# Optimization experiments

Measured on AMD Instinct MI355X. Metric: run time of the kernel, lower is better.

The kernel has to match this reference:

```python
import jax, jax.numpy as jnp
import numpy as np

B, N, D = 8, 8192, 3

def setup_inputs() -> dict:
    key = jax.random.key(0)
    k1, k2 = jax.random.split(key)
    adv_pc = jax.random.normal(k1, (B, N, D), dtype=jnp.float32)
    ori_pc = jax.random.normal(k2, (B, N, D), dtype=jnp.float32)
    weights = jnp.ones((B,), dtype=jnp.float32)
    return {"adv_pc": adv_pc, "ori_pc": ori_pc, "weights": weights}

def _batch_pairwise_dist(x, y):
    # x: [B, Nx, D], y: [B, Ny, D] -> P: [B, Nx, Ny]
    rx = jnp.sum(x * x, axis=-1)                      # [B, Nx]
    ry = jnp.sum(y * y, axis=-1)                      # [B, Ny]
    zz = jnp.einsum('bnd,bmd->bnm', x, y)             # [B, Nx, Ny]
    return rx[:, :, None] + ry[:, None, :] - 2.0 * zz

def reference(adv_pc, ori_pc, weights):
    # chamfer(preds=adv_pc, gts=ori_pc): P = pairwise(ori, adv) -> [B, N_ori, N_adv]
    P = _batch_pairwise_dist(ori_pc, adv_pc)
    loss1 = jnp.mean(jnp.min(P, axis=1), axis=1)      # adv2ori: for each adv pt, nearest ori
    # method == 'adv2ori' -> loss = loss1
    loss = loss1 * weights
    return jnp.mean(loss)
```

## Files before the change

### kernel.cpp

```cpp
#include <hip/hip_runtime.h>
#include <float.h>

#define NB 8
#define NPTS 8192
#define TOTAL (NB * NPTS)
#define BLK 256
#define WAVES 4
#define GROUPS 8
#define ADV_PER_WAVE (GROUPS * 32)
#define ADV_PER_BLOCK (WAVES * ADV_PER_WAVE)
#define ADV_BLOCKS (TOTAL / ADV_PER_BLOCK)
#define OSPLIT 16
#define OSLICE (NPTS / OSPLIT)
#define REC_SHORTS 16
#define GRID_MAIN (ADV_BLOCKS * OSPLIT)
#define BF16_ONE 0x3F80

typedef short short8 __attribute__((ext_vector_type(8)));
typedef float floatx16 __attribute__((ext_vector_type(16)));

__device__ __forceinline__ unsigned short f2bf(float f) {
    unsigned int u = __float_as_uint(f);
    return (unsigned short)((u + 0x7FFFu + ((u >> 16) & 1u)) >> 16);
}
__device__ __forceinline__ float bf2f(unsigned short h) {
    return __uint_as_float(((unsigned int)h) << 16);
}
__device__ __forceinline__ float min3(float a, float b, float c) {
    return fminf(fminf(a, b), c);
}
__device__ __forceinline__ float fold16(floatx16 d, float um) {
    float t0 = min3(d[0], d[1], d[2]);
    float t1 = min3(d[3], d[4], d[5]);
    float t2 = min3(d[6], d[7], d[8]);
    float t3 = min3(d[9], d[10], d[11]);
    float t4 = min3(d[12], d[13], d[14]);
    float t5 = min3(t0, t1, d[15]);
    float t6 = min3(t2, t3, t4);
    return min3(t5, t6, um);
}

__global__ __launch_bounds__(BLK, 4) void chamfer_mfma(const float* __restrict__ adv,
                                                       const float* __restrict__ ori,
                                                       float* __restrict__ partial) {
    __shared__ __align__(16) unsigned short lrec[OSLICE * REC_SHORTS];
    const int tid = threadIdx.x;
    const int wave = tid >> 6, lane = tid & 63;
    const int n32 = lane & 31, half = lane >> 5;
    const int advBlk = blockIdx.x >> 4;
    const int split = blockIdx.x & 15;
    const int b = advBlk >> 3;
    const int advLocal = (advBlk & 7) * ADV_PER_BLOCK + wave * ADV_PER_WAVE;

    {
        const float* orib = ori + (size_t)(b * NPTS + split * OSLICE) * 3;
#pragma unroll
        for (int r = 0; r < 2; r++) {
            int p = tid * 2 + r;
            float x = orib[3 * p + 0], y = orib[3 * p + 1], z = orib[3 * p + 2];
            unsigned short hx = f2bf(x), hy = f2bf(y), hz = f2bf(z);
            unsigned short lx = f2bf(x - bf2f(hx));
            unsigned short ly = f2bf(y - bf2f(hy));
            unsigned short lz = f2bf(z - bf2f(hz));
            float ro = fmaf(x, x, fmaf(y, y, z * z));
            unsigned short rh = f2bf(ro), rl = f2bf(ro - bf2f(rh));
            __align__(16) unsigned short rec[16] = {hx, hy, hz, lx, ly, lz, hx, hy,
                                                    hz, rh, rl, 0, 0, 0, 0, 0};
            float4* dst = (float4*)&lrec[p * REC_SHORTS];
            dst[0] = ((float4*)rec)[0];
            dst[1] = ((float4*)rec)[1];
        }
    }

    short8 bfr[GROUPS];
    float ra[GROUPS], um[GROUPS];
    const float* advb = adv + (size_t)b * NPTS * 3;
#pragma unroll
    for (int g = 0; g < GROUPS; g++) {
        int j = advLocal + g * 32 + n32;
        float x = advb[3 * j + 0], y = advb[3 * j + 1], z = advb[3 * j + 2];
        ra[g] = fmaf(x, x, fmaf(y, y, z * z));
        um[g] = FLT_MAX;
        unsigned short hx = f2bf(x), hy = f2bf(y), hz = f2bf(z);
        float fhx = bf2f(hx), fhy = bf2f(hy), fhz = bf2f(hz);
        unsigned short nhx = f2bf(-2.0f * fhx), nhy = f2bf(-2.0f * fhy), nhz = f2bf(-2.0f * fhz);
        unsigned short nlx = f2bf(-2.0f * bf2f(f2bf(x - fhx)));
        unsigned short nly = f2bf(-2.0f * bf2f(f2bf(y - fhy)));
        unsigned short nlz = f2bf(-2.0f * bf2f(f2bf(z - fhz)));
        __align__(16) unsigned short e[8] = {0, 0, 0, 0, 0, 0, 0, 0};
        if (half == 0) {
            e[0] = nhx; e[1] = nhy; e[2] = nhz;
            e[3] = nhx; e[4] = nhy; e[5] = nhz;
            e[6] = nlx; e[7] = nly;
        } else {
            e[0] = nlz; e[1] = BF16_ONE; e[2] = BF16_ONE;
        }
        bfr[g] = *(short8*)e;
    }
    __syncthreads();

    const floatx16 zero = {0.f, 0.f, 0.f, 0.f, 0.f, 0.f, 0.f, 0.f,
                           0.f, 0.f, 0.f, 0.f, 0.f, 0.f, 0.f, 0.f};
    const int lsh = n32 * REC_SHORTS + half * 8;

#pragma unroll 2
    for (int t = 0; t < OSLICE / 32; t++) {
        short8 af = *(const short8*)&lrec[t * 32 * REC_SHORTS + lsh];
#pragma unroll
        for (int g = 0; g < GROUPS; g++) {
            floatx16 d = __builtin_amdgcn_mfma_f32_32x32x16_bf16(af, bfr[g], zero, 0, 0, 0);
            um[g] = fold16(d, um[g]);
        }
    }

#pragma unroll
    for (int g = 0; g < GROUPS; g++) {
        float v = fminf(um[g], __shfl_xor(um[g], 32, 64));
        if (half == 0) {
            int col = b * NPTS + advLocal + g * 32 + n32;
            partial[(size_t)split * TOTAL + col] = ra[g] + v;
        }
    }
}

__global__ __launch_bounds__(BLK) void reduce_mins(const float* __restrict__ partial,
                                                   const float* __restrict__ w,
                                                   float* __restrict__ out) {
    const float4* p4 = (const float4*)partial;
    int g4 = blockIdx.x * BLK + threadIdx.x;
    float4 m = p4[g4];
#pragma unroll
    for (int s = 1; s < OSPLIT; s++) {
        float4 v = p4[(size_t)s * (TOTAL / 4) + g4];
        m.x = fminf(m.x, v.x); m.y = fminf(m.y, v.y);
        m.z = fminf(m.z, v.z); m.w = fminf(m.w, v.w);
    }
    float v = ((m.x + m.y) + (m.z + m.w)) * w[g4 >> 11];

    __shared__ float red[BLK];
    red[threadIdx.x] = v;
    __syncthreads();
    for (int s = BLK / 2; s > 0; s >>= 1) {
        if (threadIdx.x < s) red[threadIdx.x] += red[threadIdx.x + s];
        __syncthreads();
    }
    if (threadIdx.x == 0) atomicAdd(out, red[0] * (1.0f / (float)TOTAL));
}

extern "C" void kernel_launch(void* const* d_in, const int* in_sizes, int n_in,
                              void* d_out, int out_size, void* d_ws, size_t ws_size,
                              hipStream_t stream) {
    const float* adv = (const float*)d_in[0];
    const float* ori = (const float*)d_in[1];
    const float* w   = (const float*)d_in[2];
    float* out = (float*)d_out;
    float* partial = (float*)d_ws;

    hipMemsetAsync(out, 0, sizeof(float), stream);
    hipLaunchKernelGGL(chamfer_mfma, dim3(GRID_MAIN), dim3(BLK), 0, stream,
                       adv, ori, partial);
    hipLaunchKernelGGL(reduce_mins, dim3(TOTAL / 4 / BLK), dim3(BLK), 0, stream,
                       partial, w, out);
}
```

Before: 80.57 us.

## Drop memset, stage ori/adv loads via float4 into LDS, wave-shuffle reduce

Several changes land together. The separate memset is removed and the output is zeroed inside the main kernel. Half the block loads ori with float4 reads while the other half stages the adv block into LDS, and the adv fragments are then built from LDS. The reduce kernel shrinks to 64-thread blocks that sum with wave shuffles instead of an LDS tree. Together these aim to cut launch overhead, uncoalesced loads and synchronisation, at the cost of extra LDS use and an ordering assumption that block 0 zeroes the output before the next kernel's atomics.

```diff
diff --git a/kernel.cpp b/kernel.cpp
--- a/kernel.cpp
+++ b/kernel.cpp
@@ -42,22 +42,29 @@
 
 __global__ __launch_bounds__(BLK, 4) void chamfer_mfma(const float* __restrict__ adv,
                                                        const float* __restrict__ ori,
-                                                       float* __restrict__ partial) {
+                                                       float* __restrict__ partial,
+                                                       float* __restrict__ out) {
     __shared__ __align__(16) unsigned short lrec[OSLICE * REC_SHORTS];
+    __shared__ __align__(16) float advS[ADV_PER_BLOCK * 3];
     const int tid = threadIdx.x;
     const int wave = tid >> 6, lane = tid & 63;
     const int n32 = lane & 31, half = lane >> 5;
     const int advBlk = blockIdx.x >> 4;
     const int split = blockIdx.x & 15;
     const int b = advBlk >> 3;
-    const int advLocal = (advBlk & 7) * ADV_PER_BLOCK + wave * ADV_PER_WAVE;
+    const int advLocal = (advBlk & 7) * ADV_PER_BLOCK;
 
-    {
-        const float* orib = ori + (size_t)(b * NPTS + split * OSLICE) * 3;
+    if (blockIdx.x == 0 && tid == 0) out[0] = 0.0f;
+
+    if (tid < 128) {
+        const float4* op = (const float4*)(ori + (size_t)(b * NPTS + split * OSLICE) * 3);
+        float4 f0 = op[tid * 3 + 0], f1 = op[tid * 3 + 1], f2 = op[tid * 3 + 2];
+        float px[4] = {f0.x, f0.w, f1.z, f2.y};
+        float py[4] = {f0.y, f1.x, f1.w, f2.z};
+        float pz[4] = {f0.z, f1.y, f2.x, f2.w};
 #pragma unroll
-        for (int r = 0; r < 2; r++) {
-            int p = tid * 2 + r;
-            float x = orib[3 * p + 0], y = orib[3 * p + 1], z = orib[3 * p + 2];
+        for (int r = 0; r < 4; r++) {
+            float x = px[r], y = py[r], z = pz[r];
             unsigned short hx = f2bf(x), hy = f2bf(y), hz = f2bf(z);
             unsigned short lx = f2bf(x - bf2f(hx));
             unsigned short ly = f2bf(y - bf2f(hy));
@@ -66,19 +73,25 @@
             unsigned short rh = f2bf(ro), rl = f2bf(ro - bf2f(rh));
             __align__(16) unsigned short rec[16] = {hx, hy, hz, lx, ly, lz, hx, hy,
                                                     hz, rh, rl, 0, 0, 0, 0, 0};
-            float4* dst = (float4*)&lrec[p * REC_SHORTS];
+            float4* dst = (float4*)&lrec[(tid * 4 + r) * REC_SHORTS];
             dst[0] = ((float4*)rec)[0];
             dst[1] = ((float4*)rec)[1];
         }
+    } else {
+        const int tt = tid - 128;
+        const float4* gadv4 = (const float4*)(adv + (size_t)b * NPTS * 3 + (size_t)advLocal * 3);
+        float4* s4 = (float4*)advS;
+#pragma unroll
+        for (int i = 0; i < 6; i++) s4[tt + i * 128] = gadv4[tt + i * 128];
     }
+    __syncthreads();
 
     short8 bfr[GROUPS];
     float ra[GROUPS], um[GROUPS];
-    const float* advb = adv + (size_t)b * NPTS * 3;
 #pragma unroll
     for (int g = 0; g < GROUPS; g++) {
-        int j = advLocal + g * 32 + n32;
-        float x = advb[3 * j + 0], y = advb[3 * j + 1], z = advb[3 * j + 2];
+        int j = (wave * ADV_PER_WAVE + g * 32 + n32) * 3;
+        float x = advS[j + 0], y = advS[j + 1], z = advS[j + 2];
         ra[g] = fmaf(x, x, fmaf(y, y, z * z));
         um[g] = FLT_MAX;
         unsigned short hx = f2bf(x), hy = f2bf(y), hz = f2bf(z);
@@ -97,7 +110,6 @@
         }
         bfr[g] = *(short8*)e;
     }
-    __syncthreads();
 
     const floatx16 zero = {0.f, 0.f, 0.f, 0.f, 0.f, 0.f, 0.f, 0.f,
                            0.f, 0.f, 0.f, 0.f, 0.f, 0.f, 0.f, 0.f};
@@ -117,17 +129,17 @@
     for (int g = 0; g < GROUPS; g++) {
         float v = fminf(um[g], __shfl_xor(um[g], 32, 64));
         if (half == 0) {
-            int col = b * NPTS + advLocal + g * 32 + n32;
+            int col = b * NPTS + advLocal + wave * ADV_PER_WAVE + g * 32 + n32;
             partial[(size_t)split * TOTAL + col] = ra[g] + v;
         }
     }
 }
 
-__global__ __launch_bounds__(BLK) void reduce_mins(const float* __restrict__ partial,
-                                                   const float* __restrict__ w,
-                                                   float* __restrict__ out) {
+__global__ __launch_bounds__(64) void reduce_mins(const float* __restrict__ partial,
+                                                  const float* __restrict__ w,
+                                                  float* __restrict__ out) {
     const float4* p4 = (const float4*)partial;
-    int g4 = blockIdx.x * BLK + threadIdx.x;
+    int g4 = blockIdx.x * 64 + threadIdx.x;
     float4 m = p4[g4];
 #pragma unroll
     for (int s = 1; s < OSPLIT; s++) {
@@ -136,15 +148,9 @@
         m.z = fminf(m.z, v.z); m.w = fminf(m.w, v.w);
     }
     float v = ((m.x + m.y) + (m.z + m.w)) * w[g4 >> 11];
-
-    __shared__ float red[BLK];
-    red[threadIdx.x] = v;
-    __syncthreads();
-    for (int s = BLK / 2; s > 0; s >>= 1) {
-        if (threadIdx.x < s) red[threadIdx.x] += red[threadIdx.x + s];
-        __syncthreads();
-    }
-    if (threadIdx.x == 0) atomicAdd(out, red[0] * (1.0f / (float)TOTAL));
+#pragma unroll
+    for (int s = 32; s > 0; s >>= 1) v += __shfl_down(v, s, 64);
+    if (threadIdx.x == 0) atomicAdd(out, v * (1.0f / (float)TOTAL));
 }
 
 extern "C" void kernel_launch(void* const* d_in, const int* in_sizes, int n_in,
@@ -156,9 +162,8 @@
     float* out = (float*)d_out;
     float* partial = (float*)d_ws;
 
-    hipMemsetAsync(out, 0, sizeof(float), stream);
     hipLaunchKernelGGL(chamfer_mfma, dim3(GRID_MAIN), dim3(BLK), 0, stream,
-                       adv, ori, partial);
-    hipLaunchKernelGGL(reduce_mins, dim3(TOTAL / 4 / BLK), dim3(BLK), 0, stream,
+                       adv, ori, partial, out);
+    hipLaunchKernelGGL(reduce_mins, dim3(TOTAL / 4 / 64), dim3(64), 0, stream,
                        partial, w, out);
 }
```

Result: faster. 78.93 us (-2.0%).
